# Kernel tuning notes

Measured on AMD Instinct MI355X. Metric: run time of the kernel, lower is better.

## Reference

```python
import jax, jax.numpy as jnp
import numpy as np

N_NODES = 20000
IN_DIM = 128      # in_dim(125) + 3
HIDDEN = 256
HEADS = 3
OUT_DIM = 384
NEG_SLOPE = 0.2


def _glorot(key, shape):
    fan_in, fan_out = shape[0], shape[-1]
    lim = (6.0 / (fan_in + fan_out)) ** 0.5
    return jax.random.uniform(key, shape, jnp.float32, -lim, lim)


def setup_inputs() -> dict:
    key = jax.random.key(0)
    ks = jax.random.split(key, 12)
    x = jax.random.normal(ks[0], (N_NODES, IN_DIM), jnp.float32)
    edge_index = jax.random.randint(ks[1], (2, 320000), 0, N_NODES, jnp.int64)
    return {
        "x": x,
        "edge_index": edge_index,
        # gat1: IN_DIM -> HEADS*HIDDEN (concat)
        "W1": _glorot(ks[2], (IN_DIM, HEADS * HIDDEN)),
        "att_src1": _glorot(ks[3], (HEADS, HIDDEN)),
        "att_dst1": _glorot(ks[4], (HEADS, HIDDEN)),
        "b1": jnp.zeros((HEADS * HIDDEN,), jnp.float32),
        # gat2: HEADS*HIDDEN -> OUT_DIM (1 head)
        "W2": _glorot(ks[5], (HEADS * HIDDEN, OUT_DIM)),
        "att_src2": _glorot(ks[6], (1, OUT_DIM)),
        "att_dst2": _glorot(ks[7], (1, OUT_DIM)),
        "b2": jnp.zeros((OUT_DIM,), jnp.float32),
    }


def _gat_layer(x, src, dst, W, a_src, a_dst, bias, heads, out_ch):
    """PyG GATConv: per-head linear, LeakyReLU attention logits,
    segment-softmax over incoming edges (grouped by dst), scatter-add."""
    n = x.shape[0]
    h = (x @ W).reshape(n, heads, out_ch)               # [N,H,C]
    al_s = jnp.einsum('nhc,hc->nh', h, a_src)            # [N,H]
    al_d = jnp.einsum('nhc,hc->nh', h, a_dst)            # [N,H]
    e = jax.nn.leaky_relu(al_s[src] + al_d[dst], NEG_SLOPE)  # [E,H]
    e_max = jax.ops.segment_max(e, dst, num_segments=n)      # [N,H]
    e_exp = jnp.exp(e - e_max[dst])
    denom = jax.ops.segment_sum(e_exp, dst, num_segments=n)  # [N,H]
    alpha = e_exp / denom[dst]                               # [E,H]
    msg = h[src] * alpha[:, :, None]                         # [E,H,C]
    out = jax.ops.segment_sum(msg, dst, num_segments=n)      # [N,H,C]
    return out.reshape(n, heads * out_ch) + bias


def reference(x, edge_index, W1, att_src1, att_dst1, b1, W2, att_src2, att_dst2, b2):
    n = x.shape[0]
    # PyG GATConv default add_self_loops=True
    loops = jnp.arange(n, dtype=edge_index.dtype)
    src = jnp.concatenate([edge_index[0], loops])
    dst = jnp.concatenate([edge_index[1], loops])
    h = _gat_layer(x, src, dst, W1, att_src1, att_dst1, b1, HEADS, HIDDEN)
    h = jax.nn.relu(h)
    h = _gat_layer(h, src, dst, W2, att_src2, att_dst2, b2, 1, OUT_DIM)
    return jax.nn.relu(h)  # mode='node' -> [N, OUT_DIM]
```

## Files before the change

### kernel.cpp

```cpp
#include <hip/hip_runtime.h>
#include <hip/hip_bf16.h>

#define NEG_SLOPE 0.2f

typedef _Float16 half8 __attribute__((ext_vector_type(8)));
typedef _Float16 half4v __attribute__((ext_vector_type(4)));
typedef _Float16 half2v __attribute__((ext_vector_type(2)));
typedef float floatx4 __attribute__((ext_vector_type(4)));
typedef float floatx2 __attribute__((ext_vector_type(2)));

__global__ void k_hist(const int* __restrict__ dst, int E, int n, int* __restrict__ deg) {
    int e = blockIdx.x * blockDim.x + threadIdx.x;
    int ET = E + n;
    if (e >= ET) return;
    int d = (e < E) ? dst[e] : (e - E);
    atomicAdd(&deg[d], 1);
}

__global__ void k_scan1(const int* __restrict__ deg, int* __restrict__ bsum, int n) {
    __shared__ int red[256];
    int t = threadIdx.x, b = blockIdx.x;
    int i = b * 256 + t;
    red[t] = (i < n) ? deg[i] : 0;
    __syncthreads();
    for (int off = 128; off; off >>= 1) {
        if (t < off) red[t] += red[t + off];
        __syncthreads();
    }
    if (t == 0) bsum[b] = red[0];
}

__global__ void k_scan2(const int* __restrict__ bsum, int* __restrict__ boff, int nb) {
    __shared__ int s[256];
    int t = threadIdx.x;
    s[t] = (t < nb) ? bsum[t] : 0;
    __syncthreads();
    for (int off = 1; off < 256; off <<= 1) {
        int v = (t >= off) ? s[t - off] : 0;
        __syncthreads();
        s[t] += v;
        __syncthreads();
    }
    if (t < nb) boff[t] = (t == 0) ? 0 : s[t - 1];
}

__global__ void k_scan3(const int* __restrict__ deg, const int* __restrict__ boff,
                        int* __restrict__ rowptr, int* __restrict__ cursor, int n) {
    __shared__ int s[256];
    int t = threadIdx.x, b = blockIdx.x;
    int i = b * 256 + t;
    int v = (i < n) ? deg[i] : 0;
    s[t] = v;
    __syncthreads();
    for (int off = 1; off < 256; off <<= 1) {
        int u = (t >= off) ? s[t - off] : 0;
        __syncthreads();
        s[t] += u;
        __syncthreads();
    }
    int incl = s[t];
    int base = boff[b];
    if (i < n) {
        rowptr[i] = base + incl - v;
        cursor[i] = base + incl - v;
        if (i == n - 1) rowptr[n] = base + incl;
    }
}

__global__ void k_scatter(const int* __restrict__ src, const int* __restrict__ dst,
                          int E, int n, int* __restrict__ cursor,
                          int* __restrict__ csr_src) {
    int e = blockIdx.x * blockDim.x + threadIdx.x;
    int ET = E + n;
    if (e >= ET) return;
    int s = (e < E) ? src[e] : (e - E);
    int d = (e < E) ? dst[e] : (e - E);
    int pos = atomicAdd(&cursor[d], 1);
    csr_src[pos] = s;
}

__global__ void k_transpose_h(const float* __restrict__ W, _Float16* __restrict__ Wt,
                              int R, int C) {
    int i = blockIdx.x * 256 + threadIdx.x;
    if (i >= R * C) return;
    int c = i / R, r = i % R;
    Wt[i] = (_Float16)W[(size_t)r * C + c];
}

__global__ void k_wv1(const float* __restrict__ W1, const float* __restrict__ as1,
                      const float* __restrict__ ad1, float* __restrict__ vs,
                      float* __restrict__ vd) {
    int t = blockIdx.x * blockDim.x + threadIdx.x;
    if (t >= 384) return;
    int h = t >> 7, k = t & 127;
    const float* wr = W1 + (size_t)k * 768 + h * 256;
    const float* ar = as1 + h * 256;
    const float* dr = ad1 + h * 256;
    float s = 0.f, d = 0.f;
    for (int c = 0; c < 256; ++c) { float wv = wr[c]; s += wv * ar[c]; d += wv * dr[c]; }
    vs[t] = s; vd[t] = d;
}

__global__ void k_wv2(const float* __restrict__ W2, const float* __restrict__ as2,
                      const float* __restrict__ ad2, float* __restrict__ vs,
                      float* __restrict__ vd) {
    int t = blockIdx.x * blockDim.x + threadIdx.x;
    if (t >= 768) return;
    const float* wr = W2 + (size_t)t * 384;
    float s = 0.f, d = 0.f;
    for (int c = 0; c < 384; ++c) { float wv = wr[c]; s += wv * as2[c]; d += wv * ad2[c]; }
    vs[t] = s; vd[t] = d;
}

__global__ __launch_bounds__(256) void k_prep1(const float* __restrict__ x,
        _Float16* __restrict__ xh, const float* __restrict__ vs,
        const float* __restrict__ vd, float* __restrict__ al_s,
        float* __restrict__ al_d, int n) {
    int wid = (blockIdx.x * blockDim.x + threadIdx.x) >> 6;
    int lane = threadIdx.x & 63;
    if (wid >= n) return;
    float2 f = *(const float2*)(x + (size_t)wid * 128 + lane * 2);
    half2v hv; hv[0] = (_Float16)f.x; hv[1] = (_Float16)f.y;
    *(half2v*)(xh + (size_t)wid * 128 + lane * 2) = hv;
    float aS[3], aD[3];
#pragma unroll
    for (int hh = 0; hh < 3; ++hh) {
        floatx2 v = *(const floatx2*)(vs + hh * 128 + lane * 2);
        floatx2 d = *(const floatx2*)(vd + hh * 128 + lane * 2);
        aS[hh] = f.x * v[0] + f.y * v[1];
        aD[hh] = f.x * d[0] + f.y * d[1];
    }
#pragma unroll
    for (int hh = 0; hh < 3; ++hh)
#pragma unroll
        for (int off = 32; off; off >>= 1) {
            aS[hh] += __shfl_xor(aS[hh], off);
            aD[hh] += __shfl_xor(aD[hh], off);
        }
    if (lane == 0) {
#pragma unroll
        for (int hh = 0; hh < 3; ++hh) { al_s[wid * 3 + hh] = aS[hh]; al_d[wid * 3 + hh] = aD[hh]; }
    }
}

__global__ __launch_bounds__(256) void k_attx2(const _Float16* __restrict__ x2,
        const float* __restrict__ vs, const float* __restrict__ vd,
        float* __restrict__ al_s, float* __restrict__ al_d, int n) {
    int wid = (blockIdx.x * blockDim.x + threadIdx.x) >> 6;
    int lane = threadIdx.x & 63;
    if (wid >= n) return;
    const _Float16* xp = x2 + (size_t)wid * 768;
    half8 a = *(const half8*)(xp + lane * 8);
    half4v b = *(const half4v*)(xp + 512 + lane * 4);
    float aS = 0.f, aD = 0.f;
#pragma unroll
    for (int k = 0; k < 8; ++k) {
        float f = (float)a[k];
        aS += f * vs[lane * 8 + k];
        aD += f * vd[lane * 8 + k];
    }
#pragma unroll
    for (int k = 0; k < 4; ++k) {
        float f = (float)b[k];
        aS += f * vs[512 + lane * 4 + k];
        aD += f * vd[512 + lane * 4 + k];
    }
#pragma unroll
    for (int off = 32; off; off >>= 1) {
        aS += __shfl_xor(aS, off);
        aD += __shfl_xor(aD, off);
    }
    if (lane == 0) { al_s[wid] = aS; al_d[wid] = aD; }
}

__global__ __launch_bounds__(256) void k_aggx(const _Float16* __restrict__ xh,
                                              const float* __restrict__ al_s,
                                              const float* __restrict__ al_d,
                                              const int* __restrict__ rowptr,
                                              const int* __restrict__ csr_src,
                                              _Float16* __restrict__ xagg,
                                              int n) {
    int wid = (blockIdx.x * blockDim.x + threadIdx.x) >> 6;
    int lane = threadIdx.x & 63;
    if (wid >= n) return;
    int beg = rowptr[wid], end = rowptr[wid + 1];
    int slot = lane >> 4;
    int chunk = lane & 15;

    float ald0 = al_d[wid * 3 + 0], ald1 = al_d[wid * 3 + 1], ald2 = al_d[wid * 3 + 2];

    float acc0[8] = {}, acc1[8] = {}, acc2[8] = {};
    float sw0 = 0.f, sw1 = 0.f, sw2 = 0.f;

    for (int base = beg; base < end; base += 4) {
        int e = base + slot;
        bool v = e < end;
        int s = v ? csr_src[e] : 0;
        float w0 = 0.f, w1 = 0.f, w2 = 0.f;
        if (v) {
            float e0 = al_s[s * 3 + 0] + ald0; e0 = e0 > 0.f ? e0 : NEG_SLOPE * e0;
            float e1 = al_s[s * 3 + 1] + ald1; e1 = e1 > 0.f ? e1 : NEG_SLOPE * e1;
            float e2 = al_s[s * 3 + 2] + ald2; e2 = e2 > 0.f ? e2 : NEG_SLOPE * e2;
            w0 = __expf(e0); w1 = __expf(e1); w2 = __expf(e2);
        }
        sw0 += w0; sw1 += w1; sw2 += w2;
        half8 xv = *(const half8*)(xh + (size_t)s * 128 + chunk * 8);
#pragma unroll
        for (int k = 0; k < 8; ++k) {
            float f = (float)xv[k];
            acc0[k] = fmaf(w0, f, acc0[k]);
            acc1[k] = fmaf(w1, f, acc1[k]);
            acc2[k] = fmaf(w2, f, acc2[k]);
        }
    }
#pragma unroll
    for (int k = 0; k < 8; ++k) {
        acc0[k] += __shfl_xor(acc0[k], 16); acc0[k] += __shfl_xor(acc0[k], 32);
        acc1[k] += __shfl_xor(acc1[k], 16); acc1[k] += __shfl_xor(acc1[k], 32);
        acc2[k] += __shfl_xor(acc2[k], 16); acc2[k] += __shfl_xor(acc2[k], 32);
    }
    sw0 += __shfl_xor(sw0, 16); sw0 += __shfl_xor(sw0, 32);
    sw1 += __shfl_xor(sw1, 16); sw1 += __shfl_xor(sw1, 32);
    sw2 += __shfl_xor(sw2, 16); sw2 += __shfl_xor(sw2, 32);

    if (lane < 16) {
        float i0 = 1.f / sw0, i1 = 1.f / sw1, i2 = 1.f / sw2;
        _Float16* op = xagg + (size_t)wid * 384 + chunk * 8;
        half8 o0, o1, o2;
#pragma unroll
        for (int k = 0; k < 8; ++k) {
            o0[k] = (_Float16)(acc0[k] * i0);
            o1[k] = (_Float16)(acc1[k] * i1);
            o2[k] = (_Float16)(acc2[k] * i2);
        }
        *(half8*)(op + 0)   = o0;
        *(half8*)(op + 128) = o1;
        *(half8*)(op + 256) = o2;
    }
}

__device__ __forceinline__ void gload_lds16(const _Float16* g, _Float16* l) {
    __builtin_amdgcn_global_load_lds((const __attribute__((address_space(1))) void*)g,
                                     (__attribute__((address_space(3))) void*)l,
                                     16, 0, 0);
}

template <typename OutT, bool GAT>
__global__ __launch_bounds__(256) void k_hgemm(const _Float16* __restrict__ A,
                                               const _Float16* __restrict__ Bt,
                                               const float* __restrict__ bias,
                                               OutT* __restrict__ C,
                                               int M, int N, int K) {
    __shared__ _Float16 lds[2 * 8192];
    int t = threadIdx.x;
    int lane = t & 63, w = t >> 6;
    int wr = w >> 1, wc = w & 1;
    int lrow = lane & 15, lko = lane >> 4;
    int row0 = blockIdx.y * 128, col0 = blockIdx.x * 128;

    int sr = t & 127;
    int sko = t >> 7;
    int agr = row0 + sr; if (agr >= M) agr = M - 1;
    const _Float16* aRow;
    if constexpr (GAT) {
        int head = col0 >> 8;
        aRow = A + (size_t)agr * 384 + head * 128;
    } else {
        aRow = A + (size_t)agr * K;
    }
    const _Float16* bRow = Bt + (size_t)(col0 + sr) * K;

    floatx4 acc[4][4] = {};

    int nk = K >> 5;
#pragma unroll
    for (int s = 0; s < 2; ++s) {
        int ko = s * 2 + sko;
        gload_lds16(aRow + ko * 8, lds + s * 2048 + t * 8);
        gload_lds16(bRow + ko * 8, lds + 4096 + s * 2048 + t * 8);
    }
    __syncthreads();

    for (int ks = 0; ks < nk; ++ks) {
        int buf = ks & 1;
        if (ks + 1 < nk) {
            int kt = (ks + 1) << 5;
            _Float16* dstb = lds + (buf ^ 1) * 8192;
#pragma unroll
            for (int s = 0; s < 2; ++s) {
                int ko = s * 2 + sko;
                gload_lds16(aRow + kt + ko * 8, dstb + s * 2048 + t * 8);
                gload_lds16(bRow + kt + ko * 8, dstb + 4096 + s * 2048 + t * 8);
            }
        }
        const _Float16* base = lds + buf * 8192 + lko * 1024;
        half8 af[4], bf[4];
#pragma unroll
        for (int mi = 0; mi < 4; ++mi)
            af[mi] = *(const half8*)(base + (wr * 64 + mi * 16 + lrow) * 8);
#pragma unroll
        for (int ni = 0; ni < 4; ++ni)
            bf[ni] = *(const half8*)(base + 4096 + (wc * 64 + ni * 16 + lrow) * 8);
#pragma unroll
        for (int mi = 0; mi < 4; ++mi)
#pragma unroll
            for (int ni = 0; ni < 4; ++ni)
                acc[mi][ni] = __builtin_amdgcn_mfma_f32_16x16x32_f16(
                    af[mi], bf[ni], acc[mi][ni], 0, 0, 0);
        __syncthreads();
    }

#pragma unroll
    for (int mi = 0; mi < 4; ++mi) {
        int rb = row0 + wr * 64 + mi * 16 + lko * 4;
#pragma unroll
        for (int ni = 0; ni < 4; ++ni) {
            int col = col0 + wc * 64 + ni * 16 + lrow;
#pragma unroll
            for (int j = 0; j < 4; ++j) {
                int row = rb + j;
                if (row < M) {
                    float v = acc[mi][ni][j];
                    if constexpr (GAT) { v += bias[col]; v = v > 0.f ? v : 0.f; }
                    C[(size_t)row * N + col] = (OutT)v;
                }
            }
        }
    }
}

__global__ __launch_bounds__(256) void k_aggw2(const _Float16* __restrict__ h,
                                               const float* __restrict__ al_s,
                                               const float* __restrict__ al_d,
                                               const int* __restrict__ rowptr,
                                               const int* __restrict__ csr_src,
                                               const float* __restrict__ bias,
                                               float* __restrict__ out, int n) {
    constexpr int HC = 384;
    constexpr int CA = 4;
    constexpr int CB = 2;
    int wv = threadIdx.x >> 6;
    int lane = threadIdx.x & 63;
    int node = blockIdx.x * 2 + (wv >> 1);
    int half = wv & 1;
    int ns = wv >> 1;

    __shared__ float s_acc[2][64][CA + CB];
    __shared__ float s_sw[2];

    int beg = rowptr[node], end = rowptr[node + 1];
    float ald = al_d[node];

    float accA[CA] = {}, accB[CB] = {};
    float swsum = 0.f;

    for (int base = beg + half; base < end; base += 128) {
        int myi = base + 2 * lane;
        bool valid = myi < end;
        int sl = valid ? csr_src[myi] : 0;
        float wl = 0.f;
        if (valid) {
            float e = al_s[sl] + ald;
            e = e > 0.f ? e : NEG_SLOPE * e;
            wl = __expf(e);
        }
        swsum += wl;
        int cnt = min(64, (end - base + 1) >> 1);
        int j = 0;
        for (; j + 4 <= cnt; j += 4) {
            int ss0 = __shfl(sl, j + 0), ss1 = __shfl(sl, j + 1);
            int ss2 = __shfl(sl, j + 2), ss3 = __shfl(sl, j + 3);
            float wA0 = __shfl(wl, j + 0), wA1 = __shfl(wl, j + 1);
            float wA2 = __shfl(wl, j + 2), wA3 = __shfl(wl, j + 3);
            const _Float16* r0 = h + (size_t)ss0 * HC;
            const _Float16* r1 = h + (size_t)ss1 * HC;
            const _Float16* r2 = h + (size_t)ss2 * HC;
            const _Float16* r3 = h + (size_t)ss3 * HC;
            half4v va0 = *(const half4v*)(r0 + lane * 4);
            half4v va1 = *(const half4v*)(r1 + lane * 4);
            half4v va2 = *(const half4v*)(r2 + lane * 4);
            half4v va3 = *(const half4v*)(r3 + lane * 4);
            half2v vb0 = *(const half2v*)(r0 + 256 + lane * 2);
            half2v vb1 = *(const half2v*)(r1 + 256 + lane * 2);
            half2v vb2 = *(const half2v*)(r2 + 256 + lane * 2);
            half2v vb3 = *(const half2v*)(r3 + 256 + lane * 2);
#pragma unroll
            for (int k = 0; k < 4; ++k) {
                accA[k] = fmaf(wA0, (float)va0[k], accA[k]);
                accA[k] = fmaf(wA1, (float)va1[k], accA[k]);
                accA[k] = fmaf(wA2, (float)va2[k], accA[k]);
                accA[k] = fmaf(wA3, (float)va3[k], accA[k]);
            }
#pragma unroll
            for (int k = 0; k < 2; ++k) {
                accB[k] = fmaf(wA0, (float)vb0[k], accB[k]);
                accB[k] = fmaf(wA1, (float)vb1[k], accB[k]);
                accB[k] = fmaf(wA2, (float)vb2[k], accB[k]);
                accB[k] = fmaf(wA3, (float)vb3[k], accB[k]);
            }
        }
        for (; j < cnt; ++j) {
            int s = __shfl(sl, j);
            float aA = __shfl(wl, j);
            const _Float16* row = h + (size_t)s * HC;
            half4v va = *(const half4v*)(row + lane * 4);
            half2v vb = *(const half2v*)(row + 256 + lane * 2);
#pragma unroll
            for (int k = 0; k < 4; ++k) accA[k] = fmaf(aA, (float)va[k], accA[k]);
#pragma unroll
            for (int k = 0; k < 2; ++k) accB[k] = fmaf(aA, (float)vb[k], accB[k]);
        }
    }

#pragma unroll
    for (int off = 32; off; off >>= 1) swsum += __shfl_xor(swsum, off);

    if (half == 1) {
#pragma unroll
        for (int k = 0; k < CA; ++k) s_acc[ns][lane][k] = accA[k];
#pragma unroll
        for (int k = 0; k < CB; ++k) s_acc[ns][lane][CA + k] = accB[k];
        if (lane == 0) s_sw[ns] = swsum;
    }
    __syncthreads();
    if (half == 1) return;

#pragma unroll
    for (int k = 0; k < CA; ++k) accA[k] += s_acc[ns][lane][k];
#pragma unroll
    for (int k = 0; k < CB; ++k) accB[k] += s_acc[ns][lane][CA + k];
    float inv = 1.f / (swsum + s_sw[ns]);

    size_t obase = (size_t)node * HC;
    int cA0 = lane * CA, cB0 = 64 * CA + lane * CB;
    float4 oa;
    float t0 = accA[0] * inv + bias[cA0 + 0]; oa.x = t0 > 0.f ? t0 : 0.f;
    float t1 = accA[1] * inv + bias[cA0 + 1]; oa.y = t1 > 0.f ? t1 : 0.f;
    float t2 = accA[2] * inv + bias[cA0 + 2]; oa.z = t2 > 0.f ? t2 : 0.f;
    float t3 = accA[3] * inv + bias[cA0 + 3]; oa.w = t3 > 0.f ? t3 : 0.f;
    *(float4*)(out + obase + cA0) = oa;
    floatx2 ob;
    float u0 = accB[0] * inv + bias[cB0 + 0]; ob[0] = u0 > 0.f ? u0 : 0.f;
    float u1 = accB[1] * inv + bias[cB0 + 1]; ob[1] = u1 > 0.f ? u1 : 0.f;
    *(floatx2*)(out + obase + cB0) = ob;
}

extern "C" void kernel_launch(void* const* d_in, const int* in_sizes, int n_in,
                              void* d_out, int out_size, void* d_ws, size_t ws_size,
                              hipStream_t stream) {
    const float* x   = (const float*)d_in[0];
    const int*   ei  = (const int*)d_in[1];
    const float* W1  = (const float*)d_in[2];
    const float* as1 = (const float*)d_in[3];
    const float* ad1 = (const float*)d_in[4];
    const float* b1  = (const float*)d_in[5];
    const float* W2  = (const float*)d_in[6];
    const float* as2 = (const float*)d_in[7];
    const float* ad2 = (const float*)d_in[8];
    const float* b2  = (const float*)d_in[9];
    float* out = (float*)d_out;

    const int N  = in_sizes[0] / 128;
    const int E  = in_sizes[1] / 2;
    const int ET = E + N;
    const int NB = (N + 255) / 256;
    const int* src = ei;
    const int* dst = ei + E;

    char* ws = (char*)d_ws;
    size_t off = 0;
    auto alloc = [&](size_t bytes) {
        void* p = ws + off;
        off = (off + bytes + 255) & ~(size_t)255;
        return p;
    };
    _Float16* xh    = (_Float16*)alloc((size_t)N * 128 * 2);
    _Float16* xagg  = (_Float16*)alloc((size_t)N * 384 * 2);
    _Float16* x2h   = (_Float16*)alloc((size_t)N * 768 * 2);
    _Float16* h2    = (_Float16*)alloc((size_t)N * 384 * 2);
    _Float16* w1t   = (_Float16*)alloc((size_t)768 * 128 * 2);
    _Float16* w2t   = (_Float16*)alloc((size_t)384 * 768 * 2);
    float* vs1  = (float*)alloc(384 * 4);
    float* vd1  = (float*)alloc(384 * 4);
    float* vs2  = (float*)alloc(768 * 4);
    float* vd2  = (float*)alloc(768 * 4);
    float* alS1 = (float*)alloc((size_t)N * 3 * 4);
    float* alD1 = (float*)alloc((size_t)N * 3 * 4);
    float* alS2 = (float*)alloc((size_t)N * 4);
    float* alD2 = (float*)alloc((size_t)N * 4);
    int* deg    = (int*)alloc((size_t)N * 4);
    int* rowptr = (int*)alloc((size_t)(N + 1) * 4);
    int* cursor = (int*)alloc((size_t)N * 4);
    int* bsum   = (int*)alloc(256 * 4);
    int* boff   = (int*)alloc(256 * 4);
    int* csrs   = (int*)alloc((size_t)ET * 4);

    hipMemsetAsync(deg, 0, (size_t)N * 4, stream);
    k_hist<<<(ET + 255) / 256, 256, 0, stream>>>(dst, E, N, deg);
    k_scan1<<<NB, 256, 0, stream>>>(deg, bsum, N);
    k_scan2<<<1, 256, 0, stream>>>(bsum, boff, NB);
    k_scan3<<<NB, 256, 0, stream>>>(deg, boff, rowptr, cursor, N);
    k_scatter<<<(ET + 255) / 256, 256, 0, stream>>>(src, dst, E, N, cursor, csrs);

    k_transpose_h<<<(128 * 768 + 255) / 256, 256, 0, stream>>>(W1, w1t, 128, 768);
    k_transpose_h<<<(768 * 384 + 255) / 256, 256, 0, stream>>>(W2, w2t, 768, 384);
    k_wv1<<<2, 256, 0, stream>>>(W1, as1, ad1, vs1, vd1);
    k_wv2<<<3, 256, 0, stream>>>(W2, as2, ad2, vs2, vd2);

    k_prep1<<<(N + 3) / 4, 256, 0, stream>>>(x, xh, vs1, vd1, alS1, alD1, N);
    k_aggx<<<(N + 3) / 4, 256, 0, stream>>>(xh, alS1, alD1, rowptr, csrs, xagg, N);
    dim3 g1(768 / 128, (N + 127) / 128);
    k_hgemm<_Float16, true><<<g1, 256, 0, stream>>>(xagg, w1t, b1, x2h, N, 768, 128);

    k_attx2<<<(N + 3) / 4, 256, 0, stream>>>(x2h, vs2, vd2, alS2, alD2, N);
    dim3 g2(384 / 128, (N + 127) / 128);
    k_hgemm<_Float16, false><<<g2, 256, 0, stream>>>(x2h, w2t, nullptr, h2, N, 384, 768);
    k_aggw2<<<N / 2, 256, 0, stream>>>(h2, alS2, alD2, rowptr, csrs, b2, out, N);
}
```

Baseline: 229.4 us.

## Fuse prep kernels, compute layer-2 attention in GEMM epilogue, unroll aggregation

Merges scan2 into scan3, and merges the two weight transposes and both attention-vector kernels into one launch. The layer-2 attention logits are now computed in the first GEMM epilogue with shuffle reductions and atomics, which removes the separate pass that re-read x2. The aggregation loop handles two edges per slot per iteration to expose more memory-level parallelism. The cost is float atomics and extra registers in the GEMM epilogue, plus a shared memset covering deg and the alS2/alD2 buffers.

```diff
diff --git a/kernel.cpp b/kernel.cpp
--- a/kernel.cpp
+++ b/kernel.cpp
@@ -30,9 +30,11 @@
     if (t == 0) bsum[b] = red[0];
 }
 
-__global__ void k_scan2(const int* __restrict__ bsum, int* __restrict__ boff, int nb) {
+__global__ void k_scan3(const int* __restrict__ deg, const int* __restrict__ bsum,
+                        int nb, int* __restrict__ rowptr, int* __restrict__ cursor,
+                        int n) {
     __shared__ int s[256];
-    int t = threadIdx.x;
+    int t = threadIdx.x, b = blockIdx.x;
     s[t] = (t < nb) ? bsum[t] : 0;
     __syncthreads();
     for (int off = 1; off < 256; off <<= 1) {
@@ -41,13 +43,8 @@
         s[t] += v;
         __syncthreads();
     }
-    if (t < nb) boff[t] = (t == 0) ? 0 : s[t - 1];
-}
-
-__global__ void k_scan3(const int* __restrict__ deg, const int* __restrict__ boff,
-                        int* __restrict__ rowptr, int* __restrict__ cursor, int n) {
-    __shared__ int s[256];
-    int t = threadIdx.x, b = blockIdx.x;
+    int base = (b == 0) ? 0 : s[b - 1];
+    __syncthreads();
     int i = b * 256 + t;
     int v = (i < n) ? deg[i] : 0;
     s[t] = v;
@@ -59,7 +56,6 @@
         __syncthreads();
     }
     int incl = s[t];
-    int base = boff[b];
     if (i < n) {
         rowptr[i] = base + incl - v;
         cursor[i] = base + incl - v;
@@ -79,37 +75,41 @@
     csr_src[pos] = s;
 }
 
-__global__ void k_transpose_h(const float* __restrict__ W, _Float16* __restrict__ Wt,
-                              int R, int C) {
-    int i = blockIdx.x * 256 + threadIdx.x;
-    if (i >= R * C) return;
-    int c = i / R, r = i % R;
-    Wt[i] = (_Float16)W[(size_t)r * C + c];
-}
-
-__global__ void k_wv1(const float* __restrict__ W1, const float* __restrict__ as1,
-                      const float* __restrict__ ad1, float* __restrict__ vs,
-                      float* __restrict__ vd) {
-    int t = blockIdx.x * blockDim.x + threadIdx.x;
-    if (t >= 384) return;
-    int h = t >> 7, k = t & 127;
-    const float* wr = W1 + (size_t)k * 768 + h * 256;
-    const float* ar = as1 + h * 256;
-    const float* dr = ad1 + h * 256;
-    float s = 0.f, d = 0.f;
-    for (int c = 0; c < 256; ++c) { float wv = wr[c]; s += wv * ar[c]; d += wv * dr[c]; }
-    vs[t] = s; vd[t] = d;
-}
-
-__global__ void k_wv2(const float* __restrict__ W2, const float* __restrict__ as2,
-                      const float* __restrict__ ad2, float* __restrict__ vs,
-                      float* __restrict__ vd) {
-    int t = blockIdx.x * blockDim.x + threadIdx.x;
-    if (t >= 768) return;
-    const float* wr = W2 + (size_t)t * 384;
-    float s = 0.f, d = 0.f;
-    for (int c = 0; c < 384; ++c) { float wv = wr[c]; s += wv * as2[c]; d += wv * ad2[c]; }
-    vs[t] = s; vd[t] = d;
+__global__ void k_wprep(const float* __restrict__ W1, const float* __restrict__ W2,
+                        const float* __restrict__ as1, const float* __restrict__ ad1,
+                        const float* __restrict__ as2, const float* __restrict__ ad2,
+                        _Float16* __restrict__ w1t, _Float16* __restrict__ w2t,
+                        float* __restrict__ vs1, float* __restrict__ vd1,
+                        float* __restrict__ vs2, float* __restrict__ vd2) {
+    int b = blockIdx.x;
+    if (b < 384) {
+        int i = b * 256 + threadIdx.x;
+        int c = i / 128, r = i % 128;
+        w1t[i] = (_Float16)W1[(size_t)r * 768 + c];
+    } else if (b < 1536) {
+        int i = (b - 384) * 256 + threadIdx.x;
+        int c = i / 768, r = i % 768;
+        w2t[i] = (_Float16)W2[(size_t)r * 384 + c];
+    } else if (b < 1538) {
+        int t = (b - 1536) * 256 + threadIdx.x;
+        if (t < 384) {
+            int h = t >> 7, k = t & 127;
+            const float* wr = W1 + (size_t)k * 768 + h * 256;
+            const float* ar = as1 + h * 256;
+            const float* dr = ad1 + h * 256;
+            float s = 0.f, d = 0.f;
+            for (int c = 0; c < 256; ++c) { float wv = wr[c]; s += wv * ar[c]; d += wv * dr[c]; }
+            vs1[t] = s; vd1[t] = d;
+        }
+    } else {
+        int t = (b - 1538) * 256 + threadIdx.x;
+        if (t < 768) {
+            const float* wr = W2 + (size_t)t * 384;
+            float s = 0.f, d = 0.f;
+            for (int c = 0; c < 384; ++c) { float wv = wr[c]; s += wv * as2[c]; d += wv * ad2[c]; }
+            vs2[t] = s; vd2[t] = d;
+        }
+    }
 }
 
 __global__ __launch_bounds__(256) void k_prep1(const float* __restrict__ x,
@@ -141,36 +141,6 @@
 #pragma unroll
         for (int hh = 0; hh < 3; ++hh) { al_s[wid * 3 + hh] = aS[hh]; al_d[wid * 3 + hh] = aD[hh]; }
     }
-}
-
-__global__ __launch_bounds__(256) void k_attx2(const _Float16* __restrict__ x2,
-        const float* __restrict__ vs, const float* __restrict__ vd,
-        float* __restrict__ al_s, float* __restrict__ al_d, int n) {
-    int wid = (blockIdx.x * blockDim.x + threadIdx.x) >> 6;
-    int lane = threadIdx.x & 63;
-    if (wid >= n) return;
-    const _Float16* xp = x2 + (size_t)wid * 768;
-    half8 a = *(const half8*)(xp + lane * 8);
-    half4v b = *(const half4v*)(xp + 512 + lane * 4);
-    float aS = 0.f, aD = 0.f;
-#pragma unroll
-    for (int k = 0; k < 8; ++k) {
-        float f = (float)a[k];
-        aS += f * vs[lane * 8 + k];
-        aD += f * vd[lane * 8 + k];
-    }
-#pragma unroll
-    for (int k = 0; k < 4; ++k) {
-        float f = (float)b[k];
-        aS += f * vs[512 + lane * 4 + k];
-        aD += f * vd[512 + lane * 4 + k];
-    }
-#pragma unroll
-    for (int off = 32; off; off >>= 1) {
-        aS += __shfl_xor(aS, off);
-        aD += __shfl_xor(aD, off);
-    }
-    if (lane == 0) { al_s[wid] = aS; al_d[wid] = aD; }
 }
 
 __global__ __launch_bounds__(256) void k_aggx(const _Float16* __restrict__ xh,
@@ -192,25 +162,33 @@
     float acc0[8] = {}, acc1[8] = {}, acc2[8] = {};
     float sw0 = 0.f, sw1 = 0.f, sw2 = 0.f;
 
-    for (int base = beg; base < end; base += 4) {
-        int e = base + slot;
-        bool v = e < end;
-        int s = v ? csr_src[e] : 0;
-        float w0 = 0.f, w1 = 0.f, w2 = 0.f;
-        if (v) {
-            float e0 = al_s[s * 3 + 0] + ald0; e0 = e0 > 0.f ? e0 : NEG_SLOPE * e0;
-            float e1 = al_s[s * 3 + 1] + ald1; e1 = e1 > 0.f ? e1 : NEG_SLOPE * e1;
-            float e2 = al_s[s * 3 + 2] + ald2; e2 = e2 > 0.f ? e2 : NEG_SLOPE * e2;
-            w0 = __expf(e0); w1 = __expf(e1); w2 = __expf(e2);
-        }
-        sw0 += w0; sw1 += w1; sw2 += w2;
-        half8 xv = *(const half8*)(xh + (size_t)s * 128 + chunk * 8);
+    for (int base = beg; base < end; base += 8) {
+        int eA = base + slot, eB = base + 4 + slot;
+        bool vA = eA < end, vB = eB < end;
+        int sA = vA ? csr_src[eA] : 0;
+        int sB = vB ? csr_src[eB] : 0;
+        float wA0 = 0.f, wA1 = 0.f, wA2 = 0.f, wB0 = 0.f, wB1 = 0.f, wB2 = 0.f;
+        if (vA) {
+            float e0 = al_s[sA * 3 + 0] + ald0; e0 = e0 > 0.f ? e0 : NEG_SLOPE * e0;
+            float e1 = al_s[sA * 3 + 1] + ald1; e1 = e1 > 0.f ? e1 : NEG_SLOPE * e1;
+            float e2 = al_s[sA * 3 + 2] + ald2; e2 = e2 > 0.f ? e2 : NEG_SLOPE * e2;
+            wA0 = __expf(e0); wA1 = __expf(e1); wA2 = __expf(e2);
+        }
+        if (vB) {
+            float e0 = al_s[sB * 3 + 0] + ald0; e0 = e0 > 0.f ? e0 : NEG_SLOPE * e0;
+            float e1 = al_s[sB * 3 + 1] + ald1; e1 = e1 > 0.f ? e1 : NEG_SLOPE * e1;
+            float e2 = al_s[sB * 3 + 2] + ald2; e2 = e2 > 0.f ? e2 : NEG_SLOPE * e2;
+            wB0 = __expf(e0); wB1 = __expf(e1); wB2 = __expf(e2);
+        }
+        sw0 += wA0 + wB0; sw1 += wA1 + wB1; sw2 += wA2 + wB2;
+        half8 xvA = *(const half8*)(xh + (size_t)sA * 128 + chunk * 8);
+        half8 xvB = *(const half8*)(xh + (size_t)sB * 128 + chunk * 8);
 #pragma unroll
         for (int k = 0; k < 8; ++k) {
-            float f = (float)xv[k];
-            acc0[k] = fmaf(w0, f, acc0[k]);
-            acc1[k] = fmaf(w1, f, acc1[k]);
-            acc2[k] = fmaf(w2, f, acc2[k]);
+            float fA = (float)xvA[k], fB = (float)xvB[k];
+            acc0[k] = fmaf(wA0, fA, acc0[k]); acc0[k] = fmaf(wB0, fB, acc0[k]);
+            acc1[k] = fmaf(wA1, fA, acc1[k]); acc1[k] = fmaf(wB1, fB, acc1[k]);
+            acc2[k] = fmaf(wA2, fA, acc2[k]); acc2[k] = fmaf(wB2, fB, acc2[k]);
         }
     }
 #pragma unroll
@@ -249,6 +227,10 @@
 __global__ __launch_bounds__(256) void k_hgemm(const _Float16* __restrict__ A,
                                                const _Float16* __restrict__ Bt,
                                                const float* __restrict__ bias,
+                                               const float* __restrict__ vs2,
+                                               const float* __restrict__ vd2,
+                                               float* __restrict__ alS2,
+                                               float* __restrict__ alD2,
                                                OutT* __restrict__ C,
                                                int M, int N, int K) {
     __shared__ _Float16 lds[2 * 8192];
@@ -312,17 +294,31 @@
 
 #pragma unroll
     for (int mi = 0; mi < 4; ++mi) {
-        int rb = row0 + wr * 64 + mi * 16 + lko * 4;
-#pragma unroll
-        for (int ni = 0; ni < 4; ++ni) {
-            int col = col0 + wc * 64 + ni * 16 + lrow;
-#pragma unroll
-            for (int j = 0; j < 4; ++j) {
-                int row = rb + j;
-                if (row < M) {
-                    float v = acc[mi][ni][j];
-                    if constexpr (GAT) { v += bias[col]; v = v > 0.f ? v : 0.f; }
-                    C[(size_t)row * N + col] = (OutT)v;
+#pragma unroll
+        for (int j = 0; j < 4; ++j) {
+            int row = row0 + wr * 64 + mi * 16 + lko * 4 + j;
+            float ps = 0.f, pd = 0.f;
+#pragma unroll
+            for (int ni = 0; ni < 4; ++ni) {
+                int col = col0 + wc * 64 + ni * 16 + lrow;
+                float v = acc[mi][ni][j];
+                if constexpr (GAT) {
+                    v += bias[col]; v = v > 0.f ? v : 0.f;
+                    ps = fmaf(v, vs2[col], ps);
+                    pd = fmaf(v, vd2[col], pd);
+                }
+                if (row < M) C[(size_t)row * N + col] = (OutT)v;
+            }
+            if constexpr (GAT) {
+                if (row >= M) { ps = 0.f; pd = 0.f; }
+#pragma unroll
+                for (int off = 1; off < 16; off <<= 1) {
+                    ps += __shfl_xor(ps, off);
+                    pd += __shfl_xor(pd, off);
+                }
+                if (lrow == 0 && row < M) {
+                    atomicAdd(&alS2[row], ps);
+                    atomicAdd(&alD2[row], pd);
                 }
             }
         }
@@ -486,34 +482,33 @@
     float* vd2  = (float*)alloc(768 * 4);
     float* alS1 = (float*)alloc((size_t)N * 3 * 4);
     float* alD1 = (float*)alloc((size_t)N * 3 * 4);
+    int*   deg  = (int*)alloc((size_t)N * 4);
     float* alS2 = (float*)alloc((size_t)N * 4);
     float* alD2 = (float*)alloc((size_t)N * 4);
-    int* deg    = (int*)alloc((size_t)N * 4);
     int* rowptr = (int*)alloc((size_t)(N + 1) * 4);
     int* cursor = (int*)alloc((size_t)N * 4);
     int* bsum   = (int*)alloc(256 * 4);
-    int* boff   = (int*)alloc(256 * 4);
     int* csrs   = (int*)alloc((size_t)ET * 4);
 
-    hipMemsetAsync(deg, 0, (size_t)N * 4, stream);
+    hipMemsetAsync(deg, 0, (size_t)((char*)rowptr - (char*)deg), stream);
+
     k_hist<<<(ET + 255) / 256, 256, 0, stream>>>(dst, E, N, deg);
     k_scan1<<<NB, 256, 0, stream>>>(deg, bsum, N);
-    k_scan2<<<1, 256, 0, stream>>>(bsum, boff, NB);
-    k_scan3<<<NB, 256, 0, stream>>>(deg, boff, rowptr, cursor, N);
+    k_scan3<<<NB, 256, 0, stream>>>(deg, bsum, NB, rowptr, cursor, N);
     k_scatter<<<(ET + 255) / 256, 256, 0, stream>>>(src, dst, E, N, cursor, csrs);
 
-    k_transpose_h<<<(128 * 768 + 255) / 256, 256, 0, stream>>>(W1, w1t, 128, 768);
-    k_transpose_h<<<(768 * 384 + 255) / 256, 256, 0, stream>>>(W2, w2t, 768, 384);
-    k_wv1<<<2, 256, 0, stream>>>(W1, as1, ad1, vs1, vd1);
-    k_wv2<<<3, 256, 0, stream>>>(W2, as2, ad2, vs2, vd2);
+    k_wprep<<<1541, 256, 0, stream>>>(W1, W2, as1, ad1, as2, ad2,
+                                      w1t, w2t, vs1, vd1, vs2, vd2);
 
     k_prep1<<<(N + 3) / 4, 256, 0, stream>>>(x, xh, vs1, vd1, alS1, alD1, N);
     k_aggx<<<(N + 3) / 4, 256, 0, stream>>>(xh, alS1, alD1, rowptr, csrs, xagg, N);
     dim3 g1(768 / 128, (N + 127) / 128);
-    k_hgemm<_Float16, true><<<g1, 256, 0, stream>>>(xagg, w1t, b1, x2h, N, 768, 128);
-
-    k_attx2<<<(N + 3) / 4, 256, 0, stream>>>(x2h, vs2, vd2, alS2, alD2, N);
+    k_hgemm<_Float16, true><<<g1, 256, 0, stream>>>(xagg, w1t, b1, vs2, vd2,
+                                                    alS2, alD2, x2h, N, 768, 128);
+
     dim3 g2(384 / 128, (N + 127) / 128);
-    k_hgemm<_Float16, false><<<g2, 256, 0, stream>>>(x2h, w2t, nullptr, h2, N, 384, 768);
+    k_hgemm<_Float16, false><<<g2, 256, 0, stream>>>(x2h, w2t, nullptr, nullptr,
+                                                     nullptr, nullptr, nullptr,
+                                                     h2, N, 384, 768);
     k_aggw2<<<N / 2, 256, 0, stream>>>(h2, alS2, alD2, rowptr, csrs, b2, out, N);
 }
```

Result: faster. 211.3 us (-7.9%).
